# Optimization experiments

Hardware: AMD Instinct MI355X
Metric: run time of the kernel (lower is better)

Reference implementation:

```python
import jax, jax.numpy as jnp
import numpy as np

D_MODEL = 768
D_STATE = 16
D_CONV = 4
EXPAND = 2
D_INNER = D_MODEL * EXPAND  # 1536
B = 2
T = 8192
ALPHA = 0.9  # hard-coded EMA coefficient in _parallel_scan


def setup_inputs() -> dict:
    key = jax.random.key(0)
    ks = jax.random.split(key, 12)
    s = 0.02
    return {
        "x": jax.random.normal(ks[0], (B, T, D_MODEL), jnp.float32),
        "in_w": jax.random.normal(ks[1], (D_MODEL, 2 * D_INNER), jnp.float32) * s,
        "in_b": jnp.zeros((2 * D_INNER,), jnp.float32),
        "conv_w": jax.random.normal(ks[2], (D_INNER, 1, D_CONV), jnp.float32) * s,  # OIH, depthwise
        "conv_b": jnp.zeros((D_INNER,), jnp.float32),
        "xp_w": jax.random.normal(ks[3], (D_INNER, 2 * D_STATE), jnp.float32) * s,
        "xp_b": jnp.zeros((2 * D_STATE,), jnp.float32),
        "dt_w": jax.random.normal(ks[4], (D_STATE, D_INNER), jnp.float32) * s,
        "dt_b": jnp.zeros((D_INNER,), jnp.float32),
        "D_param": jnp.ones((D_INNER,), jnp.float32),
        "out_w": jax.random.normal(ks[5], (D_INNER, D_MODEL), jnp.float32) * s,
        "out_b": jnp.zeros((D_MODEL,), jnp.float32),
    }


def _forward(x, in_w, in_b, conv_w, conv_b, xp_w, xp_b, dt_w, dt_b, D_param, out_w, out_b):
    # in_proj: [B,T,D] -> [B,T,2*d_inner]
    xz = x @ in_w + in_b
    x_inner, z = jnp.split(xz, 2, axis=-1)

    # Causal depthwise conv1d (torch pads both sides by d_conv-1 then slices [:T],
    # which is equivalent to left-pad d_conv-1, right-pad 0)
    xc = jnp.transpose(x_inner, (0, 2, 1))  # [B, d_inner, T]
    xc = jax.lax.conv_general_dilated(
        xc, conv_w, window_strides=(1,), padding=[(D_CONV - 1, 0)],
        dimension_numbers=("NCH", "OIH", "NCH"), feature_group_count=D_INNER,
    ) + conv_b[None, :, None]
    x_conv = jax.nn.silu(jnp.transpose(xc, (0, 2, 1)))  # [B, T, d_inner]

    # NOTE: original computes x_proj/dt_proj/A_bar here, but _parallel_scan ignores
    # A_bar/B_ssm/C_ssm entirely, so they are dead code w.r.t. the output (omitted).

    # Serial EMA scan: h_t = alpha*h_{t-1} + (1-alpha)*x_conv_t
    def step(h, xt):
        h = ALPHA * h + (1.0 - ALPHA) * xt
        return h, h

    h0 = jnp.zeros((x.shape[0], D_INNER), x_conv.dtype)
    _, hs = jax.lax.scan(step, h0, jnp.transpose(x_conv, (1, 0, 2)))  # [T,B,d_inner]
    scan_out = jnp.transpose(hs, (1, 0, 2))

    y = x_conv * D_param + scan_out
    y = y * jax.nn.silu(z)
    return y @ out_w + out_b  # dropout is identity at inference


def reference(x, in_w, in_b, conv_w, conv_b, xp_w, xp_b, dt_w, dt_b, D_param, out_w, out_b):
    return _forward(x, in_w, in_b, conv_w, conv_b, xp_w, xp_b, dt_w, dt_b, D_param, out_w, out_b)
```

## Files before the change

### kernel.cpp

```cpp
#include <hip/hip_runtime.h>

#define D_MODEL 768
#define D_INNER 1536
#define NXZ     3072
#define BATCH   2
#define SEQ     8192
#define MTOT    (BATCH*SEQ)
#define WARM    64

typedef _Float16 v8h __attribute__((ext_vector_type(8)));
typedef _Float16 v4h __attribute__((ext_vector_type(4)));
typedef float    v4f __attribute__((ext_vector_type(4)));
typedef _Float16 f16;

__global__ void k_cvt(const float* __restrict__ in, f16* __restrict__ out, int n4) {
  int i = blockIdx.x * blockDim.x + threadIdx.x;
  if (i < n4) {
    float4 v = reinterpret_cast<const float4*>(in)[i];
    v4h o;
    o[0] = (f16)v.x; o[1] = (f16)v.y; o[2] = (f16)v.z; o[3] = (f16)v.w;
    reinterpret_cast<v4h*>(out)[i] = o;
  }
}

__global__ void k_transpose_cvt(const float* __restrict__ in, f16* __restrict__ out,
                                int R, int C) {
  __shared__ float tile[32][33];
  int c0 = blockIdx.x * 32, r0 = blockIdx.y * 32;
  int tx = threadIdx.x, ty = threadIdx.y;
#pragma unroll
  for (int i = 0; i < 32; i += 8)
    tile[ty + i][tx] = in[(long)(r0 + ty + i) * C + (c0 + tx)];
  __syncthreads();
#pragma unroll
  for (int i = 0; i < 32; i += 8)
    out[(long)(c0 + ty + i) * R + (r0 + tx)] = (f16)tile[tx][ty + i];
}

__device__ __forceinline__ void gload_lds16(const void* g, void* l) {
  __builtin_amdgcn_global_load_lds((const __attribute__((address_space(1))) void*)g,
                                   (__attribute__((address_space(3))) void*)l, 16, 0, 0);
}

template <bool F16OUT>
__launch_bounds__(256, 2)
__global__ void k_gemm_bt(const f16* __restrict__ A, const f16* __restrict__ Bt,
                          const float* __restrict__ bias, void* __restrict__ Cv,
                          int M, int N, int K) {
  __shared__ f16 As[128][32];
  __shared__ f16 Bs[128][32];
  const int tid  = threadIdx.x;
  const int lane = tid & 63;
  const int wave = tid >> 6;
  const int wm   = (wave >> 1) * 64;
  const int wn   = (wave & 1) * 64;
  const int m16  = lane & 15;
  const int quad = lane >> 4;
  const int rsw  = (m16 >> 1) & 3;
  const long m0 = (long)blockIdx.y * 128;
  const long n0 = (long)blockIdx.x * 128;

  v4f acc[4][4];
#pragma unroll
  for (int i = 0; i < 4; i++)
#pragma unroll
    for (int j = 0; j < 4; j++)
#pragma unroll
      for (int r = 0; r < 4; r++) acc[i][j][r] = 0.f;

  const int srow = wave * 16 + (lane >> 2);
  const int scol = (((lane & 3) ^ ((lane >> 3) & 3)) << 3);
  const f16* Ag = A  + (m0 + srow) * (long)K + scol;
  const f16* Bg = Bt + (n0 + srow) * (long)K + scol;
  f16* AsW0 = &As[wave * 16][0];
  f16* AsW1 = &As[64 + wave * 16][0];
  f16* BsW0 = &Bs[wave * 16][0];
  f16* BsW1 = &Bs[64 + wave * 16][0];

  for (int k0 = 0; k0 < K; k0 += 32) {
    gload_lds16(Ag,                 AsW0);
    gload_lds16(Ag + (long)64 * K,  AsW1);
    gload_lds16(Bg,                 BsW0);
    gload_lds16(Bg + (long)64 * K,  BsW1);
    Ag += 32; Bg += 32;
    __syncthreads();
    v8h af[4], bfr[4];
#pragma unroll
    for (int i = 0; i < 4; i++) af[i]  = *(const v8h*)&As[wm + i * 16 + m16][(quad ^ rsw) * 8];
#pragma unroll
    for (int j = 0; j < 4; j++) bfr[j] = *(const v8h*)&Bs[wn + j * 16 + m16][(quad ^ rsw) * 8];
#pragma unroll
    for (int i = 0; i < 4; i++)
#pragma unroll
      for (int j = 0; j < 4; j++)
        acc[i][j] = __builtin_amdgcn_mfma_f32_16x16x32_f16(af[i], bfr[j], acc[i][j], 0, 0, 0);
    __syncthreads();
  }

#pragma unroll
  for (int i = 0; i < 4; i++) {
#pragma unroll
    for (int j = 0; j < 4; j++) {
      const long n = n0 + wn + j * 16 + m16;
      const float bv = bias[n];
#pragma unroll
      for (int r = 0; r < 4; r++) {
        const long m = m0 + wm + i * 16 + quad * 4 + r;
        float v = acc[i][j][r] + bv;
        if (F16OUT) ((f16*)Cv)[m * N + n] = (f16)v;
        else        ((float*)Cv)[m * N + n] = v;
      }
    }
  }
}

__global__ void k_conv_scan(const f16* __restrict__ xz, const float* __restrict__ conv_w,
                            const float* __restrict__ conv_b, const float* __restrict__ Dp_,
                            f16* __restrict__ y) {
  __shared__ f16 xs[64][256];
  __shared__ f16 zs[64][256];
  const int tid = threadIdx.x;
  const int c0  = blockIdx.y * 256;
  const int c   = c0 + tid;
  const int b   = blockIdx.z;
  const int t0  = blockIdx.x * 128;
  const float w0 = conv_w[c * 4 + 0], w1 = conv_w[c * 4 + 1];
  const float w2 = conv_w[c * 4 + 2], w3 = conv_w[c * 4 + 3];
  const float cb = conv_b[c], Dp = Dp_[c];
  const long mb = (long)b * SEQ;

  float xm3 = 0.f, xm2 = 0.f, xm1 = 0.f, h = 0.f;
  const int ts = t0 - WARM;
  if (t0 > 0) {
    xm3 = (float)xz[(mb + ts - 3) * (long)NXZ + c];
    xm2 = (float)xz[(mb + ts - 2) * (long)NXZ + c];
    xm1 = (float)xz[(mb + ts - 1) * (long)NXZ + c];
  }

  for (int p = 0; p < 3; ++p) {
    const int tp = ts + p * 64;
    __syncthreads();
    if (tp >= 0) {
#pragma unroll
      for (int j = 0; j < 8; ++j) {
        const int idx = j * 256 + tid, row = idx >> 5, col = (idx & 31) << 3;
        *(v8h*)&xs[row][col] = *(const v8h*)&xz[(mb + tp + row) * (long)NXZ + c0 + col];
      }
      if (p > 0) {
#pragma unroll
        for (int j = 0; j < 8; ++j) {
          const int idx = j * 256 + tid, row = idx >> 5, col = (idx & 31) << 3;
          *(v8h*)&zs[row][col] = *(const v8h*)&xz[(mb + tp + row) * (long)NXZ + D_INNER + c0 + col];
        }
      }
    }
    __syncthreads();
    if (tp < 0) continue;
    if (p == 0) {
      for (int tl = 0; tl < 64; ++tl) {
        float xt = (float)xs[tl][tid];
        float u = w0 * xm3 + w1 * xm2 + w2 * xm1 + w3 * xt + cb;
        h = 0.9f * h + 0.1f * (u / (1.f + __expf(-u)));
        xm3 = xm2; xm2 = xm1; xm1 = xt;
      }
    } else {
      f16* yo = y + (mb + tp) * (long)D_INNER + c;
      for (int tl = 0; tl < 64; ++tl) {
        float xt = (float)xs[tl][tid];
        float u = w0 * xm3 + w1 * xm2 + w2 * xm1 + w3 * xt + cb;
        float v = u / (1.f + __expf(-u));
        h = 0.9f * h + 0.1f * v;
        float zv = (float)zs[tl][tid];
        float g = zv / (1.f + __expf(-zv));
        yo[(long)tl * D_INNER] = (f16)((v * Dp + h) * g);
        xm3 = xm2; xm2 = xm1; xm1 = xt;
      }
    }
  }
}

extern "C" void kernel_launch(void* const* d_in, const int* in_sizes, int n_in,
                              void* d_out, int out_size, void* d_ws, size_t ws_size,
                              hipStream_t stream) {
  const float* x       = (const float*)d_in[0];
  const float* in_w    = (const float*)d_in[1];
  const float* in_b    = (const float*)d_in[2];
  const float* conv_w  = (const float*)d_in[3];
  const float* conv_b  = (const float*)d_in[4];
  const float* D_param = (const float*)d_in[9];
  const float* out_w   = (const float*)d_in[10];
  const float* out_b   = (const float*)d_in[11];
  float* out = (float*)d_out;

  char* p = (char*)d_ws;
  f16* xb    = (f16*)p; p += (size_t)MTOT * D_MODEL * 2;
  f16* wInT  = (f16*)p; p += (size_t)NXZ * D_MODEL * 2;
  f16* wOutT = (f16*)p; p += (size_t)D_MODEL * D_INNER * 2;
  f16* xzb   = (f16*)p; p += (size_t)MTOT * NXZ * 2;
  f16* yb    = (f16*)p; p += (size_t)MTOT * D_INNER * 2;

  k_cvt<<<(MTOT * D_MODEL / 4 + 255) / 256, 256, 0, stream>>>(x, xb, MTOT * D_MODEL / 4);
  k_transpose_cvt<<<dim3(NXZ / 32, D_MODEL / 32), dim3(32, 8), 0, stream>>>(in_w, wInT, D_MODEL, NXZ);
  k_transpose_cvt<<<dim3(D_MODEL / 32, D_INNER / 32), dim3(32, 8), 0, stream>>>(out_w, wOutT, D_INNER, D_MODEL);

  k_gemm_bt<true><<<dim3(NXZ / 128, MTOT / 128), 256, 0, stream>>>(xb, wInT, in_b, xzb, MTOT, NXZ, D_MODEL);

  k_conv_scan<<<dim3(SEQ / 128, D_INNER / 256, BATCH), 256, 0, stream>>>(xzb, conv_w, conv_b, D_param, yb);

  k_gemm_bt<false><<<dim3(D_MODEL / 128, MTOT / 128), 256, 0, stream>>>(yb, wOutT, out_b, out, MTOT, D_MODEL, D_INNER);
}
```

Baseline: 349.1 us.

## Replace GEMM with 256x256 tiled, double-buffered, ping-pong scheduled MFMA kernel

Replaces the 128x128 single-buffered GEMM with a 256x256 tile, 512-thread kernel. It double-buffers K-slices in LDS using global_load_lds and interleaves LDS reads, async stages and MFMA blocks with explicit barriers, setprio and waitcnt control. It also adds an XCD-aware workgroup swizzle to improve L2 locality. The goal is to hide global-load latency, raise arithmetic intensity per tile and cut barrier stalls in both projections. In exchange it uses much more LDS and registers (128 accumulators per lane), and the small grid for the output GEMM (3x64 tiles) may underfill the device.

```diff
diff --git a/kernel.cpp b/kernel.cpp
--- a/kernel.cpp
+++ b/kernel.cpp
@@ -43,75 +43,136 @@
 }
 
 template <bool F16OUT>
-__launch_bounds__(256, 2)
-__global__ void k_gemm_bt(const f16* __restrict__ A, const f16* __restrict__ Bt,
+__launch_bounds__(512, 2)
+__global__ void k_gemm256(const f16* __restrict__ A, const f16* __restrict__ Bt,
                           const float* __restrict__ bias, void* __restrict__ Cv,
                           int M, int N, int K) {
-  __shared__ f16 As[128][32];
-  __shared__ f16 Bs[128][32];
+  __shared__ f16 sA[2][2][8192];
+  __shared__ f16 sB[2][2][8192];
   const int tid  = threadIdx.x;
   const int lane = tid & 63;
   const int wave = tid >> 6;
-  const int wm   = (wave >> 1) * 64;
-  const int wn   = (wave & 1) * 64;
+  const int wm   = wave >> 2;
+  const int wn   = wave & 3;
   const int m16  = lane & 15;
   const int quad = lane >> 4;
-  const int rsw  = (m16 >> 1) & 3;
-  const long m0 = (long)blockIdx.y * 128;
-  const long n0 = (long)blockIdx.x * 128;
-
-  v4f acc[4][4];
-#pragma unroll
-  for (int i = 0; i < 4; i++)
-#pragma unroll
-    for (int j = 0; j < 4; j++)
-#pragma unroll
-      for (int r = 0; r < 4; r++) acc[i][j][r] = 0.f;
-
-  const int srow = wave * 16 + (lane >> 2);
-  const int scol = (((lane & 3) ^ ((lane >> 3) & 3)) << 3);
-  const f16* Ag = A  + (m0 + srow) * (long)K + scol;
-  const f16* Bg = Bt + (n0 + srow) * (long)K + scol;
-  f16* AsW0 = &As[wave * 16][0];
-  f16* AsW1 = &As[64 + wave * 16][0];
-  f16* BsW0 = &Bs[wave * 16][0];
-  f16* BsW1 = &Bs[64 + wave * 16][0];
-
-  for (int k0 = 0; k0 < K; k0 += 32) {
-    gload_lds16(Ag,                 AsW0);
-    gload_lds16(Ag + (long)64 * K,  AsW1);
-    gload_lds16(Bg,                 BsW0);
-    gload_lds16(Bg + (long)64 * K,  BsW1);
-    Ag += 32; Bg += 32;
-    __syncthreads();
-    v8h af[4], bfr[4];
-#pragma unroll
-    for (int i = 0; i < 4; i++) af[i]  = *(const v8h*)&As[wm + i * 16 + m16][(quad ^ rsw) * 8];
-#pragma unroll
-    for (int j = 0; j < 4; j++) bfr[j] = *(const v8h*)&Bs[wn + j * 16 + m16][(quad ^ rsw) * 8];
-#pragma unroll
-    for (int i = 0; i < 4; i++)
-#pragma unroll
-      for (int j = 0; j < 4; j++)
-        acc[i][j] = __builtin_amdgcn_mfma_f32_16x16x32_f16(af[i], bfr[j], acc[i][j], 0, 0, 0);
-    __syncthreads();
-  }
-
-#pragma unroll
-  for (int i = 0; i < 4; i++) {
-#pragma unroll
-    for (int j = 0; j < 4; j++) {
-      const long n = n0 + wn + j * 16 + m16;
+
+  const int nwg  = gridDim.x * gridDim.y;
+  const int orig = blockIdx.y * gridDim.x + blockIdx.x;
+  const int swz  = (orig & 7) * (nwg >> 3) + (orig >> 3);
+  const int bx   = swz % gridDim.x;
+  const int by   = swz / gridDim.x;
+  const long m0  = (long)by * 256;
+  const long n0  = (long)bx * 256;
+
+  const int  srow = wave * 16 + m16;
+  const int  scol = quad * 8;
+  const f16* aS0 = A  + (m0 + srow) * (long)K + scol;
+  const f16* aS1 = aS0 + (long)128 * K;
+  const f16* bS0 = Bt + (n0 + srow) * (long)K + scol;
+  const f16* bS1 = bS0 + (long)128 * K;
+
+#define STG_A(b_, kp_, ko_)                                        \
+  gload_lds16(aS0 + (ko_), &sA[b_][kp_][wave << 9]);               \
+  gload_lds16(aS1 + (ko_), &sA[b_][kp_][(8 + wave) << 9]);
+#define STG_B(b_, kp_, ko_)                                        \
+  gload_lds16(bS0 + (ko_), &sB[b_][kp_][wave << 9]);               \
+  gload_lds16(bS1 + (ko_), &sB[b_][kp_][(8 + wave) << 9]);
+#define RD_A(b_, kp_, miB_)                                                          \
+  fa[0] = *(const v8h*)&sA[b_][kp_][(((wm << 3) + (miB_) + 0) << 9) + (lane << 3)];  \
+  fa[1] = *(const v8h*)&sA[b_][kp_][(((wm << 3) + (miB_) + 1) << 9) + (lane << 3)];  \
+  fa[2] = *(const v8h*)&sA[b_][kp_][(((wm << 3) + (miB_) + 2) << 9) + (lane << 3)];  \
+  fa[3] = *(const v8h*)&sA[b_][kp_][(((wm << 3) + (miB_) + 3) << 9) + (lane << 3)];
+#define RD_B(b_, kp_)                                                                \
+  fb[0] = *(const v8h*)&sB[b_][kp_][(((wn << 2) + 0) << 9) + (lane << 3)];           \
+  fb[1] = *(const v8h*)&sB[b_][kp_][(((wn << 2) + 1) << 9) + (lane << 3)];           \
+  fb[2] = *(const v8h*)&sB[b_][kp_][(((wn << 2) + 2) << 9) + (lane << 3)];           \
+  fb[3] = *(const v8h*)&sB[b_][kp_][(((wn << 2) + 3) << 9) + (lane << 3)];
+#define MMQ(miB_, i_)                                                                              \
+  acc[(miB_)+i_][0] = __builtin_amdgcn_mfma_f32_16x16x32_f16(fa[i_], fb[0], acc[(miB_)+i_][0], 0, 0, 0); \
+  acc[(miB_)+i_][1] = __builtin_amdgcn_mfma_f32_16x16x32_f16(fa[i_], fb[1], acc[(miB_)+i_][1], 0, 0, 0); \
+  acc[(miB_)+i_][2] = __builtin_amdgcn_mfma_f32_16x16x32_f16(fa[i_], fb[2], acc[(miB_)+i_][2], 0, 0, 0); \
+  acc[(miB_)+i_][3] = __builtin_amdgcn_mfma_f32_16x16x32_f16(fa[i_], fb[3], acc[(miB_)+i_][3], 0, 0, 0);
+#define MM(miB_)                                          \
+  __builtin_amdgcn_s_barrier();                           \
+  asm volatile("s_waitcnt lgkmcnt(0)" ::: "memory");      \
+  __builtin_amdgcn_sched_barrier(0);                      \
+  __builtin_amdgcn_s_setprio(1);                          \
+  MMQ(miB_, 0) MMQ(miB_, 1) MMQ(miB_, 2) MMQ(miB_, 3)     \
+  __builtin_amdgcn_s_setprio(0);                          \
+  __builtin_amdgcn_sched_barrier(0);                      \
+  __builtin_amdgcn_s_barrier();
+
+  v4f acc[8][4];
+#pragma unroll
+  for (int i = 0; i < 8; ++i)
+#pragma unroll
+    for (int j = 0; j < 4; ++j)
+#pragma unroll
+      for (int r = 0; r < 4; ++r) acc[i][j][r] = 0.f;
+  v8h fa[4], fb[4];
+
+  const int T = K >> 6;
+
+  STG_A(0, 0, 0)  STG_B(0, 0, 0)
+  STG_A(0, 1, 32) STG_B(0, 1, 32)
+  STG_A(1, 0, 64) STG_B(1, 0, 64)
+  asm volatile("s_waitcnt vmcnt(4)" ::: "memory");
+  __builtin_amdgcn_s_barrier();
+
+  int t = 0;
+#pragma unroll 1
+  for (; t < T - 2; ++t) {
+    const int b  = t & 1, nb = b ^ 1;
+    const int k1 = (t + 1) * 64 + 32;
+    const int k2 = (t + 2) * 64;
+    RD_B(b, 0) RD_A(b, 0, 0) STG_A(nb, 1, k1) MM(0)
+    RD_A(b, 0, 4)            STG_B(nb, 1, k1) MM(4)
+    RD_B(b, 1) RD_A(b, 1, 0) STG_A(b, 0, k2)  MM(0)
+    RD_A(b, 1, 4)            STG_B(b, 0, k2)
+    asm volatile("s_waitcnt vmcnt(4)" ::: "memory");
+    MM(4)
+  }
+  {
+    const int b  = t & 1, nb = b ^ 1;
+    const int k1 = (t + 1) * 64 + 32;
+    RD_B(b, 0) RD_A(b, 0, 0) STG_A(nb, 1, k1) MM(0)
+    RD_A(b, 0, 4)            STG_B(nb, 1, k1) MM(4)
+    RD_B(b, 1) RD_A(b, 1, 0)                  MM(0)
+    RD_A(b, 1, 4)
+    asm volatile("s_waitcnt vmcnt(0)" ::: "memory");
+    MM(4)
+    ++t;
+  }
+  {
+    const int b = t & 1;
+    RD_B(b, 0) RD_A(b, 0, 0) MM(0)
+    RD_A(b, 0, 4)            MM(4)
+    RD_B(b, 1) RD_A(b, 1, 0) MM(0)
+    RD_A(b, 1, 4)            MM(4)
+  }
+
+#pragma unroll
+  for (int i = 0; i < 8; ++i) {
+#pragma unroll
+    for (int j = 0; j < 4; ++j) {
+      const long n = n0 + wn * 64 + j * 16 + m16;
       const float bv = bias[n];
 #pragma unroll
-      for (int r = 0; r < 4; r++) {
-        const long m = m0 + wm + i * 16 + quad * 4 + r;
+      for (int r = 0; r < 4; ++r) {
+        const long m = m0 + wm * 128 + i * 16 + quad * 4 + r;
         float v = acc[i][j][r] + bv;
         if (F16OUT) ((f16*)Cv)[m * N + n] = (f16)v;
         else        ((float*)Cv)[m * N + n] = v;
       }
     }
   }
+#undef STG_A
+#undef STG_B
+#undef RD_A
+#undef RD_B
+#undef MMQ
+#undef MM
 }
 
 __global__ void k_conv_scan(const f16* __restrict__ xz, const float* __restrict__ conv_w,
@@ -203,9 +264,9 @@
   k_transpose_cvt<<<dim3(NXZ / 32, D_MODEL / 32), dim3(32, 8), 0, stream>>>(in_w, wInT, D_MODEL, NXZ);
   k_transpose_cvt<<<dim3(D_MODEL / 32, D_INNER / 32), dim3(32, 8), 0, stream>>>(out_w, wOutT, D_INNER, D_MODEL);
 
-  k_gemm_bt<true><<<dim3(NXZ / 128, MTOT / 128), 256, 0, stream>>>(xb, wInT, in_b, xzb, MTOT, NXZ, D_MODEL);
+  k_gemm256<true><<<dim3(NXZ / 256, MTOT / 256), 512, 0, stream>>>(xb, wInT, in_b, xzb, MTOT, NXZ, D_MODEL);
 
   k_conv_scan<<<dim3(SEQ / 128, D_INNER / 256, BATCH), 256, 0, stream>>>(xzb, conv_w, conv_b, D_param, yb);
 
-  k_gemm_bt<false><<<dim3(D_MODEL / 128, MTOT / 128), 256, 0, stream>>>(yb, wOutT, out_b, out, MTOT, D_MODEL, D_INNER);
-}
+  k_gemm256<false><<<dim3(D_MODEL / 256, MTOT / 256), 512, 0, stream>>>(yb, wOutT, out_b, out, MTOT, D_MODEL, D_INNER);
+}
```

Result: slower. 368.3 us (+5.5%).
